# Kernel optimization log

Hardware: AMD Instinct MI355X
Metric: run time of the kernel (lower is better)

The kernel has to match this reference:

```python
import jax, jax.numpy as jnp
import numpy as np


def setup_inputs() -> dict:
    key = jax.random.key(0)
    ks = jax.random.split(key, 5)
    N_IN, N_OUT, RANK, W, T = 128, 64, 10, 101, 50000
    X = jax.random.normal(ks[0], (N_IN, T), dtype=jnp.float32)
    # K: (rank, 2, window); channel axis = (real, imag) parts of complex kernels.
    K = jax.random.normal(ks[1], (RANK, 2, W), dtype=jnp.float32) * 0.1
    B1 = jax.random.normal(ks[2], (N_IN, RANK), dtype=jnp.float32) * 0.1
    B2 = jax.random.normal(ks[3], (RANK, N_OUT), dtype=jnp.float32) * 0.1
    bias = jax.random.normal(ks[4], (N_OUT, 1), dtype=jnp.float32) * 0.1
    return {"X": X, "K": K, "B1": B1, "B2": B2, "bias": bias}


def reference(X, K, B1, B2, bias):
    # X: (n, T) real; K: (rank, 2, W) -> complex kernels (rank, W)
    T = X.shape[-1]
    W = K.shape[-1]
    n_fft = T + W - 1
    Kc = (K[:, 0, :] + 1j * K[:, 1, :]).astype(jnp.complex64)
    # fftconvolve along last dim, broadcasting (n,1,*) x (1,rank,*)
    Xf = jnp.fft.fft(X[:, None, :], n=n_fft, axis=-1)          # (n, 1, n_fft)
    Kf = jnp.fft.fft(Kc[None, :, :], n=n_fft, axis=-1)         # (1, rank, n_fft)
    conv_full = jnp.fft.ifft(Xf * Kf, axis=-1)                 # (n, rank, n_fft)
    # mode='same' with odd W: start = ceil((n_fft - T)/2) = (W-1)//2
    start = (W - 1) // 2
    c = jnp.abs(conv_full[..., start:start + T])               # (n, rank, T) real
    # standardize over time with unbiased std (torch.std default, ddof=1)
    mean = jnp.mean(c, axis=2, keepdims=True)
    d = c - mean
    std = jnp.sqrt(jnp.sum(d * d, axis=2, keepdims=True) / (T - 1))
    z = d / std
    # low-rank readout: 'nkt,nk,km->mt' then bias (broadcast over t)
    out = jnp.einsum('nkt,nk,km->mt', z, B1, B2) + bias        # (m, T)
    return out
```

## Files before the change

### kernel.cpp

```cpp
#include <hip/hip_runtime.h>
#include <hip/hip_bf16.h>

#define NIN   128
#define NOUT  64
#define RANK  10
#define WLEN  101
#define TLEN  50000
#define TILE  512
#define NTT   98
#define TPAD  (NTT * TILE)
#define NA    51
#define XS    616
#define KLDS  (NA * 20)
#define RLEN  648
#define CBOFF 561

typedef _Float16 h2 __attribute__((ext_vector_type(2)));
typedef _Float16 half8 __attribute__((ext_vector_type(8)));
typedef float f32x4 __attribute__((ext_vector_type(4)));

__device__ __forceinline__ h2 as_h2(unsigned u) {
    union { unsigned x; h2 h; } c; c.x = u; return c.h;
}
__device__ __forceinline__ unsigned packh(float lo, float hi) {
    union { h2 h; unsigned u; } c;
    c.h.x = (_Float16)lo; c.h.y = (_Float16)hi; return c.u;
}
__device__ __forceinline__ unsigned short h16(float v) {
    union { _Float16 h; unsigned short u; } c;
    c.h = (_Float16)v; return c.u;
}

#if defined(__has_builtin)
#if __has_builtin(__builtin_amdgcn_fdot2)
#define FDOT2(a, b, c) __builtin_amdgcn_fdot2((a), (b), (c), false)
#endif
#endif
#ifndef FDOT2
__device__ __forceinline__ float fdot2_sw(h2 a, h2 b, float c) {
    return fmaf((float)a.x, (float)b.x, fmaf((float)a.y, (float)b.y, c));
}
#define FDOT2(a, b, c) fdot2_sw((a), (b), (c))
#endif

__global__ void k_prep_taps(const float* __restrict__ K, _Float16* __restrict__ Af) {
    int idx = blockIdx.x * 256 + threadIdx.x;
    if (idx >= 32 * 128) return;
    int row = idx >> 7, j = idx & 127;
    int rank = row >> 1, comp = row & 1;
    float v = (rank < RANK && j < WLEN) ? K[(rank * 2 + comp) * WLEN + j] : 0.f;
    Af[idx] = (_Float16)v;
}

__global__ void k_prep(const float* __restrict__ K, unsigned* __restrict__ Kd2) {
    int idx = blockIdx.x * 256 + threadIdx.x;
    if (idx >= KLDS) return;
    int a = idx / 20, r = idx % 20;
    int k = r >> 1, comp = r & 1;
    int j0 = 2 * a, j1 = 2 * a + 1;
    float v0 = K[(k * 2 + comp) * WLEN + j0];
    float v1 = (j1 < WLEN) ? K[(k * 2 + comp) * WLEN + j1] : 0.f;
    Kd2[idx] = packh(v0, v1);
}

template <int STORE_C>
__global__ __launch_bounds__(256, 2) void k_conv(
        const float* __restrict__ X,
        const _Float16* __restrict__ Af,
        unsigned short* __restrict__ chs,
        float* __restrict__ sums,
        float* __restrict__ sumsq) {
    __shared__ __align__(16) _Float16 R[RLEN];
    __shared__ __align__(16) _Float16 RS[8][RLEN];
    __shared__ float red1[4][RANK], red2[4][RANK];
    const int n = blockIdx.y, tile = blockIdx.x, tid = threadIdx.x;
    const int t0 = tile * TILE;
    const float* Xn = X + (size_t)n * TLEN;

    for (int p = tid; p < RLEN; p += 256) {
        int xi = t0 + CBOFF - p;
        R[p] = (xi >= 0 && xi < TLEN) ? (_Float16)Xn[xi] : (_Float16)0.f;
    }
    __syncthreads();
#pragma unroll 1
    for (int s = 0; s < 8; ++s)
        for (int i = tid; i < RLEN; i += 256)
            RS[s][i] = (i + s < RLEN) ? R[i + s] : (_Float16)0.f;
    __syncthreads();

    const int lane = tid & 63, wid = tid >> 6;
    const int c = lane & 15, q0 = lane >> 4;
    const int s = (7 - c) & 7;
    const int ra = 2 * q0;

    const half8* Ap = (const half8*)Af;
    half8 a0[4], a1[4];
#pragma unroll
    for (int ks = 0; ks < 4; ++ks) {
        a0[ks] = Ap[c * 16 + 4 * ks + q0];
        a1[ks] = Ap[(16 + c) * 16 + 4 * ks + q0];
    }
    const half8* Bp = (const half8*)&RS[s][0];

    float sa0 = 0, sb0 = 0, sa1 = 0, sb1 = 0;
    float sa2 = 0, sb2 = 0, sa3 = 0, sb3 = 0;
#pragma unroll 1
    for (int it = 0; it < 8; ++it) {
        const int tau = wid * 8 + it;
        const int base8 = (511 - 16 * tau + 8 * q0 - c - s) >> 3;
        f32x4 acc0 = {0.f, 0.f, 0.f, 0.f};
        f32x4 acc1 = {0.f, 0.f, 0.f, 0.f};
#pragma unroll
        for (int ks = 0; ks < 4; ++ks) {
            half8 b = Bp[base8 + 4 * ks];
            acc0 = __builtin_amdgcn_mfma_f32_16x16x32_f16(a0[ks], b, acc0, 0, 0, 0);
            acc1 = __builtin_amdgcn_mfma_f32_16x16x32_f16(a1[ks], b, acc1, 0, 0, 0);
        }
        float m00 = sqrtf(fmaf(acc0[0], acc0[0], acc0[1] * acc0[1]));
        float m01 = sqrtf(fmaf(acc0[2], acc0[2], acc0[3] * acc0[3]));
        float m10 = sqrtf(fmaf(acc1[0], acc1[0], acc1[1] * acc1[1]));
        float m11 = sqrtf(fmaf(acc1[2], acc1[2], acc1[3] * acc1[3]));
        int t = t0 + 16 * tau + c;
        float v0 = (t < TLEN) ? m00 : 0.f;
        float v1 = (t < TLEN) ? m01 : 0.f;
        float v2 = (t < TLEN) ? m10 : 0.f;
        float v3 = (t < TLEN) ? m11 : 0.f;
        sa0 += v0; sb0 = fmaf(v0, v0, sb0);
        sa1 += v1; sb1 = fmaf(v1, v1, sb1);
        sa2 += v2; sb2 = fmaf(v2, v2, sb2);
        sa3 += v3; sb3 = fmaf(v3, v3, sb3);
        if (STORE_C) {
            size_t tt = (size_t)t;
            chs[((size_t)(n * RANK + ra)) * TPAD + tt] = h16(m00);
            chs[((size_t)(n * RANK + ra + 1)) * TPAD + tt] = h16(m01);
            if (q0 == 0) {
                chs[((size_t)(n * RANK + 8)) * TPAD + tt] = h16(m10);
                chs[((size_t)(n * RANK + 9)) * TPAD + tt] = h16(m11);
            }
        }
    }
#pragma unroll
    for (int m = 1; m <= 8; m <<= 1) {
        sa0 += __shfl_xor(sa0, m); sb0 += __shfl_xor(sb0, m);
        sa1 += __shfl_xor(sa1, m); sb1 += __shfl_xor(sb1, m);
        sa2 += __shfl_xor(sa2, m); sb2 += __shfl_xor(sb2, m);
        sa3 += __shfl_xor(sa3, m); sb3 += __shfl_xor(sb3, m);
    }
    if (c == 0) {
        red1[wid][ra] = sa0;     red2[wid][ra] = sb0;
        red1[wid][ra + 1] = sa1; red2[wid][ra + 1] = sb1;
        if (q0 == 0) {
            red1[wid][8] = sa2; red2[wid][8] = sb2;
            red1[wid][9] = sa3; red2[wid][9] = sb3;
        }
    }
    __syncthreads();
    if (tid < RANK) {
        float a = red1[0][tid] + red1[1][tid] + red1[2][tid] + red1[3][tid];
        atomicAdd(&sums[n * RANK + tid], a);
    } else if (tid >= 64 && tid < 64 + RANK) {
        int k = tid - 64;
        float b = red2[0][k] + red2[1][k] + red2[2][k] + red2[3][k];
        atomicAdd(&sumsq[n * RANK + k], b);
    }
}

__global__ void k_fin(const float* __restrict__ sums,
                      const float* __restrict__ sumsq,
                      const float* __restrict__ B1,
                      const float* __restrict__ B2,
                      const float* __restrict__ bias,
                      float* __restrict__ Wm,
                      float* __restrict__ bias2) {
    __shared__ float mw[NIN * RANK];
    int tid = threadIdx.x;
    for (int idx = tid; idx < NIN * RANK; idx += 256) {
        float s = sums[idx], s2 = sumsq[idx];
        float mean = s / (float)TLEN;
        float var = fmaxf((s2 - s * mean) / (float)(TLEN - 1), 1e-12f);
        float w = B1[idx] / sqrtf(var);
        Wm[idx] = w;
        mw[idx] = mean * w;
    }
    __syncthreads();
    if (tid < NOUT) {
        float acc = bias[tid];
        for (int n = 0; n < NIN; ++n)
#pragma unroll
            for (int k = 0; k < RANK; ++k)
                acc -= mw[n * RANK + k] * B2[k * NOUT + tid];
        bias2[tid] = acc;
    }
}

__global__ void k_comb(const unsigned* __restrict__ ch,
                       const float* __restrict__ Wm,
                       float* __restrict__ ypart, int npc) {
    __shared__ float wl[NIN * RANK / 4];
    int t2 = blockIdx.x * 256 + threadIdx.x;
    int chn = blockIdx.y, tid = threadIdx.x;
    int n0 = chn * npc;
    for (int idx = tid; idx < npc * RANK; idx += 256)
        wl[idx] = Wm[n0 * RANK + idx];
    __syncthreads();
    float2 y[RANK];
#pragma unroll
    for (int k = 0; k < RANK; ++k) y[k] = make_float2(0.f, 0.f);
    for (int nn = 0; nn < npc; ++nn) {
#pragma unroll
        for (int k = 0; k < RANK; ++k) {
            unsigned u = ch[((size_t)((n0 + nn) * RANK + k)) * (TPAD >> 1) + t2];
            h2 v = as_h2(u);
            float w = wl[nn * RANK + k];
            y[k].x = fmaf((float)v.x, w, y[k].x);
            y[k].y = fmaf((float)v.y, w, y[k].y);
        }
    }
#pragma unroll
    for (int k = 0; k < RANK; ++k)
        *(float2*)&ypart[((size_t)(chn * RANK + k)) * TPAD + 2 * t2] = y[k];
}

__device__ __forceinline__ void stage_Rp(const float* __restrict__ Xn,
                                         unsigned* Rs, int tstart) {
    for (int p = threadIdx.x; p < XS; p += 256) {
        int s = tstart - 55 + p;
        float x0 = (s >= 0 && s < TLEN) ? Xn[s] : 0.f;
        float x1 = (s + 1 >= 0 && s + 1 < TLEN) ? Xn[s + 1] : 0.f;
        Rs[p] = packh(x1, x0);
    }
}

__device__ __forceinline__ void conv_all(const unsigned* Rs, const unsigned* Kl,
                                         int tid,
                                         float (&re)[RANK][2],
                                         float (&im)[RANK][2]) {
#pragma unroll
    for (int k = 0; k < RANK; ++k) {
        re[k][0] = 0.f; re[k][1] = 0.f; im[k][0] = 0.f; im[k][1] = 0.f;
    }
    int pb = 2 * tid + 104;
#pragma unroll 1
    for (int ap = 0; ap < 25; ++ap) {
        int p = pb - 4 * ap;
        uint2 wA = *(const uint2*)&Rs[p];
        uint2 wB = *(const uint2*)&Rs[p - 2];
        h2 e0 = as_h2(wA.x), e1 = as_h2(wA.y);
        h2 o0 = as_h2(wB.x), o1 = as_h2(wB.y);
        const uint4* t0 = (const uint4*)&Kl[40 * ap];
        const uint4* t1 = (const uint4*)&Kl[40 * ap + 20];
#pragma unroll
        for (int kp = 0; kp < 5; ++kp) {
            const int k0 = 2 * kp, k1 = 2 * kp + 1;
            uint4 ta = t0[kp];
            h2 r0 = as_h2(ta.x), i0 = as_h2(ta.y);
            h2 r1 = as_h2(ta.z), i1 = as_h2(ta.w);
            re[k0][0] = FDOT2(e0, r0, re[k0][0]); im[k0][0] = FDOT2(e0, i0, im[k0][0]);
            re[k0][1] = FDOT2(e1, r0, re[k0][1]); im[k0][1] = FDOT2(e1, i0, im[k0][1]);
            re[k1][0] = FDOT2(e0, r1, re[k1][0]); im[k1][0] = FDOT2(e0, i1, im[k1][0]);
            re[k1][1] = FDOT2(e1, r1, re[k1][1]); im[k1][1] = FDOT2(e1, i1, im[k1][1]);
            uint4 tb = t1[kp];
            h2 s0 = as_h2(tb.x), j0 = as_h2(tb.y);
            h2 s1 = as_h2(tb.z), j1 = as_h2(tb.w);
            re[k0][0] = FDOT2(o0, s0, re[k0][0]); im[k0][0] = FDOT2(o0, j0, im[k0][0]);
            re[k0][1] = FDOT2(o1, s0, re[k0][1]); im[k0][1] = FDOT2(o1, j0, im[k0][1]);
            re[k1][0] = FDOT2(o0, s1, re[k1][0]); im[k1][0] = FDOT2(o0, j1, im[k1][0]);
            re[k1][1] = FDOT2(o1, s1, re[k1][1]); im[k1][1] = FDOT2(o1, j1, im[k1][1]);
        }
    }
    {
        int p = pb - 100;
        uint2 wA = *(const uint2*)&Rs[p];
        h2 e0 = as_h2(wA.x), e1 = as_h2(wA.y);
        const uint4* t0 = (const uint4*)&Kl[1000];
#pragma unroll
        for (int kp = 0; kp < 5; ++kp) {
            const int k0 = 2 * kp, k1 = 2 * kp + 1;
            uint4 ta = t0[kp];
            h2 r0 = as_h2(ta.x), i0 = as_h2(ta.y);
            h2 r1 = as_h2(ta.z), i1 = as_h2(ta.w);
            re[k0][0] = FDOT2(e0, r0, re[k0][0]); im[k0][0] = FDOT2(e0, i0, im[k0][0]);
            re[k0][1] = FDOT2(e1, r0, re[k0][1]); im[k0][1] = FDOT2(e1, i0, im[k0][1]);
            re[k1][0] = FDOT2(e0, r1, re[k1][0]); im[k1][0] = FDOT2(e0, i1, im[k1][0]);
            re[k1][1] = FDOT2(e1, r1, re[k1][1]); im[k1][1] = FDOT2(e1, i1, im[k1][1]);
        }
    }
}

__global__ __launch_bounds__(256, 4) void k_comb_re(const float* __restrict__ X,
                          const unsigned* __restrict__ Kd2,
                          const float* __restrict__ Wm,
                          float* __restrict__ ypart, int npc) {
    __shared__ __align__(16) unsigned Rs[XS];
    __shared__ __align__(16) unsigned Kl[KLDS];
    int chn = blockIdx.y, tile = blockIdx.x, tid = threadIdx.x;
    int tstart = tile * TILE;
    for (int idx = tid; idx < KLDS; idx += 256) Kl[idx] = Kd2[idx];
    float y[RANK][2];
#pragma unroll
    for (int k = 0; k < RANK; ++k) { y[k][0] = 0.f; y[k][1] = 0.f; }
    int n0 = chn * npc;
#pragma unroll 1
    for (int nn = 0; nn < npc; ++nn) {
        int n = n0 + nn;
        stage_Rp(X + (size_t)n * TLEN, Rs, tstart);
        __syncthreads();
        float re[RANK][2], im[RANK][2];
        conv_all(Rs, Kl, tid, re, im);
#pragma unroll
        for (int k = 0; k < RANK; ++k) {
            float w = Wm[n * RANK + k];
            float v0 = sqrtf(fmaf(re[k][0], re[k][0], im[k][0] * im[k][0]));
            float v1 = sqrtf(fmaf(re[k][1], re[k][1], im[k][1] * im[k][1]));
            y[k][0] = fmaf(v0, w, y[k][0]);
            y[k][1] = fmaf(v1, w, y[k][1]);
        }
        __syncthreads();
    }
    int tb = tstart + 2 * tid;
#pragma unroll
    for (int k = 0; k < RANK; ++k)
        *(float2*)&ypart[((size_t)(chn * RANK + k)) * TPAD + tb] =
            make_float2(y[k][0], y[k][1]);
}

__global__ void k_out(const float* __restrict__ ypart,
                      const float* __restrict__ B2,
                      const float* __restrict__ bias2,
                      float* __restrict__ out, int nch) {
    int t2 = blockIdx.x * 256 + threadIdx.x;
    int t = 2 * t2;
    if (t >= TLEN) return;
    float2 y[RANK];
#pragma unroll
    for (int k = 0; k < RANK; ++k) y[k] = make_float2(0.f, 0.f);
    for (int chn = 0; chn < nch; ++chn) {
#pragma unroll
        for (int k = 0; k < RANK; ++k) {
            float2 v = *(const float2*)&ypart[((size_t)(chn * RANK + k)) * TPAD + t];
            y[k].x += v.x;
            y[k].y += v.y;
        }
    }
    for (int m = 0; m < NOUT; ++m) {
        float b = bias2[m];
        float2 acc = make_float2(b, b);
#pragma unroll
        for (int k = 0; k < RANK; ++k) {
            float w = B2[k * NOUT + m];
            acc.x = fmaf(y[k].x, w, acc.x);
            acc.y = fmaf(y[k].y, w, acc.y);
        }
        *(float2*)&out[(size_t)m * TLEN + t] = acc;
    }
}

extern "C" void kernel_launch(void* const* d_in, const int* in_sizes, int n_in,
                              void* d_out, int out_size, void* d_ws, size_t ws_size,
                              hipStream_t stream) {
    const float* X    = (const float*)d_in[0];
    const float* K    = (const float*)d_in[1];
    const float* B1   = (const float*)d_in[2];
    const float* B2   = (const float*)d_in[3];
    const float* bias = (const float*)d_in[4];
    float* out = (float*)d_out;

    char* p = (char*)d_ws;
    size_t off = 0;
    auto alloc = [&](size_t bytes) -> void* {
        void* r = p + off;
        off += (bytes + 255) & ~(size_t)255;
        return r;
    };
    float* sums  = (float*)alloc(NIN * RANK * sizeof(float));
    float* sumsq = (float*)alloc(NIN * RANK * sizeof(float));
    float* Wm    = (float*)alloc(NIN * RANK * sizeof(float));
    float* bias2 = (float*)alloc(NOUT * sizeof(float));
    unsigned* Kd2 = (unsigned*)alloc(KLDS * sizeof(unsigned));
    _Float16* Af  = (_Float16*)alloc(32 * 128 * sizeof(_Float16));

    size_t cbytes = (size_t)NIN * RANK * TPAD * sizeof(unsigned short);
    auto ypb = [](int n) {
        return (((size_t)n * RANK * TPAD * sizeof(float)) + 255) & ~(size_t)255;
    };

    int mode, nch;
    if (ws_size >= off + ypb(8) + cbytes)      { mode = 0; nch = 8; }
    else if (ws_size >= off + ypb(4) + cbytes) { mode = 0; nch = 4; }
    else if (ws_size >= off + ypb(8))          { mode = 1; nch = 8; }
    else                                       { mode = 1; nch = 1; }

    float* ypart = (float*)alloc((size_t)nch * RANK * TPAD * sizeof(float));
    unsigned short* c = (unsigned short*)(p + off);

    hipMemsetAsync(sums, 0, 2 * NIN * RANK * sizeof(float), stream);

    k_prep_taps<<<dim3(16), 256, 0, stream>>>(K, Af);
    if (mode == 1)
        k_prep<<<dim3((KLDS + 255) / 256), 256, 0, stream>>>(K, Kd2);

    if (mode == 0)
        k_conv<1><<<dim3(NTT, NIN), 256, 0, stream>>>(X, Af, c, sums, sumsq);
    else
        k_conv<0><<<dim3(NTT, NIN), 256, 0, stream>>>(X, Af, c, sums, sumsq);

    k_fin<<<1, 256, 0, stream>>>(sums, sumsq, B1, B2, bias, Wm, bias2);

    if (mode == 0) {
        k_comb<<<dim3(NTT, nch), 256, 0, stream>>>((const unsigned*)c, Wm, ypart, NIN / nch);
    } else {
        k_comb_re<<<dim3(NTT, nch), 256, 0, stream>>>(X, Kd2, Wm, ypart, NIN / nch);
    }

    k_out<<<dim3(TPAD / 512), 256, 0, stream>>>(ypart, B2, bias2, out, nch);
}
```

Baseline: 223.5 us.

## Pack rank-pair magnitudes, stage shifted rows directly, split tail tile, cache B2

```diff
diff --git a/kernel.cpp b/kernel.cpp
--- a/kernel.cpp
+++ b/kernel.cpp
@@ -4,32 +4,29 @@
 #define NIN   128
 #define NOUT  64
 #define RANK  10
+#define NPAIR 5
 #define WLEN  101
 #define TLEN  50000
 #define TILE  512
 #define NTT   98
 #define TPAD  (NTT * TILE)
+#define CBOFF 561
+#define RROW  648
+#define RROWD 324
 #define NA    51
 #define XS    616
 #define KLDS  (NA * 20)
-#define RLEN  648
-#define CBOFF 561
 
 typedef _Float16 h2 __attribute__((ext_vector_type(2)));
 typedef _Float16 half8 __attribute__((ext_vector_type(8)));
 typedef float f32x4 __attribute__((ext_vector_type(4)));
 
-__device__ __forceinline__ h2 as_h2(unsigned u) {
-    union { unsigned x; h2 h; } c; c.x = u; return c.h;
-}
-__device__ __forceinline__ unsigned packh(float lo, float hi) {
-    union { h2 h; unsigned u; } c;
-    c.h.x = (_Float16)lo; c.h.y = (_Float16)hi; return c.u;
-}
-__device__ __forceinline__ unsigned short h16(float v) {
-    union { _Float16 h; unsigned short u; } c;
-    c.h = (_Float16)v; return c.u;
-}
+__device__ __forceinline__ unsigned pk_rne(float lo, float hi) {
+    h2 v; v.x = (_Float16)lo; v.y = (_Float16)hi;
+    return __builtin_bit_cast(unsigned, v);
+}
+__device__ __forceinline__ unsigned packh(float lo, float hi) { return pk_rne(lo, hi); }
+__device__ __forceinline__ h2 as_h2(unsigned u) { return __builtin_bit_cast(h2, u); }
 
 #if defined(__has_builtin)
 #if __has_builtin(__builtin_amdgcn_fdot2)
@@ -63,35 +60,43 @@
     Kd2[idx] = packh(v0, v1);
 }
 
-template <int STORE_C>
-__global__ __launch_bounds__(256, 2) void k_conv(
-        const float* __restrict__ X,
-        const _Float16* __restrict__ Af,
-        unsigned short* __restrict__ chs,
-        float* __restrict__ sums,
+template <bool TAIL, bool STORE>
+__global__ __launch_bounds__(256, 4) void k_conv(
+        const float* __restrict__ X, const _Float16* __restrict__ Af,
+        unsigned* __restrict__ c4, float* __restrict__ sums,
         float* __restrict__ sumsq) {
-    __shared__ __align__(16) _Float16 R[RLEN];
-    __shared__ __align__(16) _Float16 RS[8][RLEN];
+    __shared__ __align__(16) _Float16 RS[8][RROW];
     __shared__ float red1[4][RANK], red2[4][RANK];
-    const int n = blockIdx.y, tile = blockIdx.x, tid = threadIdx.x;
+    const int n = blockIdx.y, tid = threadIdx.x;
+    const int tile = TAIL ? (NTT - 1) : blockIdx.x;
     const int t0 = tile * TILE;
     const float* Xn = X + (size_t)n * TLEN;
-
-    for (int p = tid; p < RLEN; p += 256) {
-        int xi = t0 + CBOFF - p;
-        R[p] = (xi >= 0 && xi < TLEN) ? (_Float16)Xn[xi] : (_Float16)0.f;
-    }
-    __syncthreads();
-#pragma unroll 1
-    for (int s = 0; s < 8; ++s)
-        for (int i = tid; i < RLEN; i += 256)
-            RS[s][i] = (i + s < RLEN) ? R[i + s] : (_Float16)0.f;
+    const int C = t0 + CBOFF;
+
+    unsigned* RSd = (unsigned*)&RS[0][0];
+    if (TAIL || tile == 0) {
+#pragma unroll
+        for (int s = 0; s < 8; ++s)
+            for (int d = tid; d < RROWD; d += 256) {
+                int i0 = C - 2 * d - 1 - s;
+                float a = (i0 >= 0 && i0 < TLEN) ? Xn[i0] : 0.f;
+                float b = (i0 + 1 >= 0 && i0 + 1 < TLEN) ? Xn[i0 + 1] : 0.f;
+                RSd[s * RROWD + d] = pk_rne(b, a);
+            }
+    } else {
+#pragma unroll
+        for (int s = 0; s < 8; ++s)
+            for (int d = tid; d < RROWD; d += 256) {
+                int i0 = C - 2 * d - 1 - s;
+                float a = Xn[i0], b = Xn[i0 + 1];
+                RSd[s * RROWD + d] = pk_rne(b, a);
+            }
+    }
     __syncthreads();
 
     const int lane = tid & 63, wid = tid >> 6;
     const int c = lane & 15, q0 = lane >> 4;
     const int s = (7 - c) & 7;
-    const int ra = 2 * q0;
 
     const half8* Ap = (const half8*)Af;
     half8 a0[4], a1[4];
@@ -100,44 +105,51 @@
         a0[ks] = Ap[c * 16 + 4 * ks + q0];
         a1[ks] = Ap[(16 + c) * 16 + 4 * ks + q0];
     }
-    const half8* Bp = (const half8*)&RS[s][0];
+
+    const int Q = ((511 + 8 * q0 - c - s) >> 3) - 16 * wid - 14;
+    const char* vbase = (const char*)RS + s * 1296 + 16 * Q;
+
+    const int tbase = t0 + 128 * wid + c;
+    unsigned* st0 = c4 + (size_t)(n * NPAIR + q0) * TPAD + tbase;
+    unsigned* st1 = c4 + (size_t)(n * NPAIR + 4) * TPAD + tbase;
 
     float sa0 = 0, sb0 = 0, sa1 = 0, sb1 = 0;
     float sa2 = 0, sb2 = 0, sa3 = 0, sb3 = 0;
-#pragma unroll 1
+    float m10v[8], m11v[8];
+
+#pragma unroll
     for (int it = 0; it < 8; ++it) {
-        const int tau = wid * 8 + it;
-        const int base8 = (511 - 16 * tau + 8 * q0 - c - s) >> 3;
         f32x4 acc0 = {0.f, 0.f, 0.f, 0.f};
         f32x4 acc1 = {0.f, 0.f, 0.f, 0.f};
 #pragma unroll
         for (int ks = 0; ks < 4; ++ks) {
-            half8 b = Bp[base8 + 4 * ks];
+            half8 b = *(const half8*)(vbase + 32 * (7 - it) + 64 * ks);
             acc0 = __builtin_amdgcn_mfma_f32_16x16x32_f16(a0[ks], b, acc0, 0, 0, 0);
             acc1 = __builtin_amdgcn_mfma_f32_16x16x32_f16(a1[ks], b, acc1, 0, 0, 0);
         }
-        float m00 = sqrtf(fmaf(acc0[0], acc0[0], acc0[1] * acc0[1]));
-        float m01 = sqrtf(fmaf(acc0[2], acc0[2], acc0[3] * acc0[3]));
-        float m10 = sqrtf(fmaf(acc1[0], acc1[0], acc1[1] * acc1[1]));
-        float m11 = sqrtf(fmaf(acc1[2], acc1[2], acc1[3] * acc1[3]));
-        int t = t0 + 16 * tau + c;
-        float v0 = (t < TLEN) ? m00 : 0.f;
-        float v1 = (t < TLEN) ? m01 : 0.f;
-        float v2 = (t < TLEN) ? m10 : 0.f;
-        float v3 = (t < TLEN) ? m11 : 0.f;
-        sa0 += v0; sb0 = fmaf(v0, v0, sb0);
-        sa1 += v1; sb1 = fmaf(v1, v1, sb1);
-        sa2 += v2; sb2 = fmaf(v2, v2, sb2);
-        sa3 += v3; sb3 = fmaf(v3, v3, sb3);
-        if (STORE_C) {
-            size_t tt = (size_t)t;
-            chs[((size_t)(n * RANK + ra)) * TPAD + tt] = h16(m00);
-            chs[((size_t)(n * RANK + ra + 1)) * TPAD + tt] = h16(m01);
-            if (q0 == 0) {
-                chs[((size_t)(n * RANK + 8)) * TPAD + tt] = h16(m10);
-                chs[((size_t)(n * RANK + 9)) * TPAD + tt] = h16(m11);
-            }
-        }
+        float rr00 = fmaf(acc0[0], acc0[0], acc0[1] * acc0[1]);
+        float rr01 = fmaf(acc0[2], acc0[2], acc0[3] * acc0[3]);
+        float rr10 = fmaf(acc1[0], acc1[0], acc1[1] * acc1[1]);
+        float rr11 = fmaf(acc1[2], acc1[2], acc1[3] * acc1[3]);
+        float m00 = sqrtf(rr00), m01 = sqrtf(rr01);
+        float m10 = sqrtf(rr10), m11 = sqrtf(rr11);
+        if (TAIL) {
+            float g = (tbase + 16 * it < TLEN) ? 1.f : 0.f;
+            sa0 = fmaf(g, m00, sa0); sb0 = fmaf(g, rr00, sb0);
+            sa1 = fmaf(g, m01, sa1); sb1 = fmaf(g, rr01, sb1);
+            sa2 = fmaf(g, m10, sa2); sb2 = fmaf(g, rr10, sb2);
+            sa3 = fmaf(g, m11, sa3); sb3 = fmaf(g, rr11, sb3);
+        } else {
+            sa0 += m00; sb0 += rr00; sa1 += m01; sb1 += rr01;
+            sa2 += m10; sb2 += rr10; sa3 += m11; sb3 += rr11;
+        }
+        m10v[it] = m10; m11v[it] = m11;
+        if (STORE) st0[16 * it] = pk_rne(m00, m01);
+    }
+    if (STORE && q0 == 0) {
+#pragma unroll
+        for (int it = 0; it < 8; ++it)
+            st1[16 * it] = pk_rne(m10v[it], m11v[it]);
     }
 #pragma unroll
     for (int m = 1; m <= 8; m <<= 1) {
@@ -147,8 +159,8 @@
         sa3 += __shfl_xor(sa3, m); sb3 += __shfl_xor(sb3, m);
     }
     if (c == 0) {
-        red1[wid][ra] = sa0;     red2[wid][ra] = sb0;
-        red1[wid][ra + 1] = sa1; red2[wid][ra + 1] = sb1;
+        red1[wid][2 * q0] = sa0;     red2[wid][2 * q0] = sb0;
+        red1[wid][2 * q0 + 1] = sa1; red2[wid][2 * q0 + 1] = sb1;
         if (q0 == 0) {
             red1[wid][8] = sa2; red2[wid][8] = sb2;
             red1[wid][9] = sa3; red2[wid][9] = sb3;
@@ -156,12 +168,12 @@
     }
     __syncthreads();
     if (tid < RANK) {
-        float a = red1[0][tid] + red1[1][tid] + red1[2][tid] + red1[3][tid];
-        atomicAdd(&sums[n * RANK + tid], a);
+        atomicAdd(&sums[n * RANK + tid],
+                  red1[0][tid] + red1[1][tid] + red1[2][tid] + red1[3][tid]);
     } else if (tid >= 64 && tid < 64 + RANK) {
         int k = tid - 64;
-        float b = red2[0][k] + red2[1][k] + red2[2][k] + red2[3][k];
-        atomicAdd(&sumsq[n * RANK + k], b);
+        atomicAdd(&sumsq[n * RANK + k],
+                  red2[0][k] + red2[1][k] + red2[2][k] + red2[3][k]);
     }
 }
 
@@ -193,32 +205,37 @@
     }
 }
 
-__global__ void k_comb(const unsigned* __restrict__ ch,
-                       const float* __restrict__ Wm,
-                       float* __restrict__ ypart, int npc) {
-    __shared__ float wl[NIN * RANK / 4];
-    int t2 = blockIdx.x * 256 + threadIdx.x;
-    int chn = blockIdx.y, tid = threadIdx.x;
-    int n0 = chn * npc;
-    for (int idx = tid; idx < npc * RANK; idx += 256)
-        wl[idx] = Wm[n0 * RANK + idx];
+__global__ __launch_bounds__(256, 4) void k_comb(
+        const unsigned* __restrict__ c4, const float* __restrict__ Wm,
+        float* __restrict__ ypart) {
+    __shared__ float wl[16 * RANK];
+    const int tid = threadIdx.x, ch = blockIdx.y;
+    const int n0 = ch * 16;
+    if (tid < 16 * RANK) wl[tid] = Wm[n0 * RANK + tid];
     __syncthreads();
+    const int t = 2 * (blockIdx.x * 256 + tid);
+    const unsigned* pr = c4 + (size_t)(n0 * NPAIR) * TPAD + t;
     float2 y[RANK];
 #pragma unroll
     for (int k = 0; k < RANK; ++k) y[k] = make_float2(0.f, 0.f);
-    for (int nn = 0; nn < npc; ++nn) {
-#pragma unroll
-        for (int k = 0; k < RANK; ++k) {
-            unsigned u = ch[((size_t)((n0 + nn) * RANK + k)) * (TPAD >> 1) + t2];
-            h2 v = as_h2(u);
-            float w = wl[nn * RANK + k];
-            y[k].x = fmaf((float)v.x, w, y[k].x);
-            y[k].y = fmaf((float)v.y, w, y[k].y);
+#pragma unroll 2
+    for (int nn = 0; nn < 16; ++nn) {
+#pragma unroll
+        for (int p = 0; p < NPAIR; ++p) {
+            uint2 u = *(const uint2*)pr;
+            pr += TPAD;
+            h2 v0 = as_h2(u.x);
+            h2 v1 = as_h2(u.y);
+            float2 w = *(const float2*)&wl[nn * RANK + 2 * p];
+            y[2 * p].x     = fmaf(w.x, (float)v0.x, y[2 * p].x);
+            y[2 * p].y     = fmaf(w.x, (float)v1.x, y[2 * p].y);
+            y[2 * p + 1].x = fmaf(w.y, (float)v0.y, y[2 * p + 1].x);
+            y[2 * p + 1].y = fmaf(w.y, (float)v1.y, y[2 * p + 1].y);
         }
     }
 #pragma unroll
     for (int k = 0; k < RANK; ++k)
-        *(float2*)&ypart[((size_t)(chn * RANK + k)) * TPAD + 2 * t2] = y[k];
+        *(float2*)&ypart[(size_t)(ch * RANK + k) * TPAD + t] = y[k];
 }
 
 __device__ __forceinline__ void stage_Rp(const float* __restrict__ Xn,
@@ -324,34 +341,38 @@
             make_float2(y[k][0], y[k][1]);
 }
 
-__global__ void k_out(const float* __restrict__ ypart,
+__global__ __launch_bounds__(256, 2) void k_out(const float* __restrict__ ypart,
                       const float* __restrict__ B2,
                       const float* __restrict__ bias2,
                       float* __restrict__ out, int nch) {
-    int t2 = blockIdx.x * 256 + threadIdx.x;
-    int t = 2 * t2;
-    if (t >= TLEN) return;
+    __shared__ float b2l[RANK * NOUT];
+    __shared__ float bl[NOUT];
+    const int tid = threadIdx.x;
+    for (int i = tid; i < RANK * NOUT; i += 256) b2l[i] = B2[i];
+    if (tid < NOUT) bl[tid] = bias2[tid];
+    __syncthreads();
+    const int t = 2 * (blockIdx.x * 256 + tid);
     float2 y[RANK];
 #pragma unroll
     for (int k = 0; k < RANK; ++k) y[k] = make_float2(0.f, 0.f);
-    for (int chn = 0; chn < nch; ++chn) {
+    for (int ch = 0; ch < nch; ++ch)
 #pragma unroll
         for (int k = 0; k < RANK; ++k) {
-            float2 v = *(const float2*)&ypart[((size_t)(chn * RANK + k)) * TPAD + t];
-            y[k].x += v.x;
-            y[k].y += v.y;
-        }
-    }
-    for (int m = 0; m < NOUT; ++m) {
-        float b = bias2[m];
-        float2 acc = make_float2(b, b);
-#pragma unroll
-        for (int k = 0; k < RANK; ++k) {
-            float w = B2[k * NOUT + m];
-            acc.x = fmaf(y[k].x, w, acc.x);
-            acc.y = fmaf(y[k].y, w, acc.y);
-        }
-        *(float2*)&out[(size_t)m * TLEN + t] = acc;
+            float2 v = *(const float2*)&ypart[(size_t)(ch * RANK + k) * TPAD + t];
+            y[k].x += v.x; y[k].y += v.y;
+        }
+    if (t < TLEN) {
+#pragma unroll 1
+        for (int m = 0; m < NOUT; ++m) {
+            float ax = bl[m], ay = bl[m];
+#pragma unroll
+            for (int k = 0; k < RANK; ++k) {
+                float w = b2l[k * NOUT + m];
+                ax = fmaf(w, y[k].x, ax);
+                ay = fmaf(w, y[k].y, ay);
+            }
+            *(float2*)&out[(size_t)m * TLEN + t] = make_float2(ax, ay);
+        }
     }
 }
 
@@ -379,19 +400,18 @@
     unsigned* Kd2 = (unsigned*)alloc(KLDS * sizeof(unsigned));
     _Float16* Af  = (_Float16*)alloc(32 * 128 * sizeof(_Float16));
 
-    size_t cbytes = (size_t)NIN * RANK * TPAD * sizeof(unsigned short);
+    size_t cbytes = (size_t)NIN * NPAIR * TPAD * sizeof(unsigned);
     auto ypb = [](int n) {
         return (((size_t)n * RANK * TPAD * sizeof(float)) + 255) & ~(size_t)255;
     };
 
     int mode, nch;
-    if (ws_size >= off + ypb(8) + cbytes)      { mode = 0; nch = 8; }
-    else if (ws_size >= off + ypb(4) + cbytes) { mode = 0; nch = 4; }
-    else if (ws_size >= off + ypb(8))          { mode = 1; nch = 8; }
-    else                                       { mode = 1; nch = 1; }
+    if (ws_size >= off + ypb(8) + cbytes) { mode = 0; nch = 8; }
+    else if (ws_size >= off + ypb(8))     { mode = 1; nch = 8; }
+    else                                  { mode = 1; nch = 1; }
 
     float* ypart = (float*)alloc((size_t)nch * RANK * TPAD * sizeof(float));
-    unsigned short* c = (unsigned short*)(p + off);
+    unsigned* c4 = (unsigned*)(p + off);
 
     hipMemsetAsync(sums, 0, 2 * NIN * RANK * sizeof(float), stream);
 
@@ -399,18 +419,21 @@
     if (mode == 1)
         k_prep<<<dim3((KLDS + 255) / 256), 256, 0, stream>>>(K, Kd2);
 
-    if (mode == 0)
-        k_conv<1><<<dim3(NTT, NIN), 256, 0, stream>>>(X, Af, c, sums, sumsq);
-    else
-        k_conv<0><<<dim3(NTT, NIN), 256, 0, stream>>>(X, Af, c, sums, sumsq);
+    if (mode == 0) {
+        k_conv<false, true><<<dim3(NTT - 1, NIN), 256, 0, stream>>>(X, Af, c4, sums, sumsq);
+        k_conv<true, true><<<dim3(1, NIN), 256, 0, stream>>>(X, Af, c4, sums, sumsq);
+    } else {
+        k_conv<false, false><<<dim3(NTT - 1, NIN), 256, 0, stream>>>(X, Af, c4, sums, sumsq);
+        k_conv<true, false><<<dim3(1, NIN), 256, 0, stream>>>(X, Af, c4, sums, sumsq);
+    }
 
     k_fin<<<1, 256, 0, stream>>>(sums, sumsq, B1, B2, bias, Wm, bias2);
 
     if (mode == 0) {
-        k_comb<<<dim3(NTT, nch), 256, 0, stream>>>((const unsigned*)c, Wm, ypart, NIN / nch);
+        k_comb<<<dim3(TPAD / 512, 8), 256, 0, stream>>>(c4, Wm, ypart);
+        k_out<<<dim3(TPAD / 512), 256, 0, stream>>>(ypart, B2, bias2, out, 8);
     } else {
         k_comb_re<<<dim3(NTT, nch), 256, 0, stream>>>(X, Kd2, Wm, ypart, NIN / nch);
-    }
-
-    k_out<<<dim3(TPAD / 512), 256, 0, stream>>>(ypart, B2, bias2, out, nch);
-}
+        k_out<<<dim3(TPAD / 512), 256, 0, stream>>>(ypart, B2, bias2, out, nch);
+    }
+}
```

Result: slower. 253.5 us (+13.4%).
